# Kernel optimization log

Hardware: AMD Instinct MI355X
Metric: run time of the kernel (lower is better)

The kernel has to match this reference:

```python
import jax, jax.numpy as jnp
import numpy as np

NUM_CLASSES = 19
IGNORE_INDEX = 255
FOCAL_GAMMA = 3.0
FOCAL_WEIGHT = 1.0
EPS = 1e-6


def setup_inputs() -> dict:
    key = jax.random.key(0)
    k1, k2 = jax.random.split(key)
    logits = jax.random.normal(k1, (8, NUM_CLASSES, 512, 512), dtype=jnp.float32)
    targets = jax.random.randint(k2, (8, 512, 512), 0, NUM_CLASSES, dtype=jnp.int64)
    return {"logits": logits, "targets": targets}


def reference(logits, targets):
    C = NUM_CLASSES
    # [B,C,H,W] -> [N,C] log-probs, N = B*H*W
    logp = jax.nn.log_softmax(logits, axis=1)
    lp = jnp.transpose(logp, (0, 2, 3, 1)).reshape(-1, C)
    t = targets.reshape(-1)
    valid = (t != IGNORE_INDEX)
    tc = jnp.clip(t, 0, C - 1)  # safe index for ignored pixels
    validf = valid.astype(lp.dtype)
    n_valid = jnp.maximum(jnp.sum(validf), 1.0)

    # mean cross entropy over valid pixels (F.cross_entropy with ignore_index)
    nll = -jnp.take_along_axis(lp, tc[:, None], axis=1)[:, 0]
    ce = jnp.sum(nll * validf) / n_valid

    # per-class focal term: -log(p_t) * (1 - p_t)^gamma, p_t clamped to [1e-6, 1]
    pt = jnp.clip(jnp.exp(-nll), EPS, 1.0)
    focal_terms = -jnp.log(pt) * (1.0 - pt) ** FOCAL_GAMMA

    # single-pass segment reduce: per-class sum and count over valid pixels
    sums = jax.ops.segment_sum(focal_terms * validf, tc, num_segments=C)
    counts = jax.ops.segment_sum(validf, tc, num_segments=C)
    present = counts > 0
    per_class_mean = sums / jnp.maximum(counts, 1.0)
    n_present = jnp.maximum(jnp.sum(present.astype(lp.dtype)), 1.0)
    focal = jnp.sum(jnp.where(present, per_class_mean, 0.0)) / n_present

    return ce + FOCAL_WEIGHT * focal
```

## Files before the change

kernel.cpp:

```cpp
#include <hip/hip_runtime.h>


#define NCLS 19
#define IGNORE_IDX 255
#define HW4 65536
#define FOCAL_EPS 1e-6f
#define NBLK 2048
#define NQ 40
#define TILE4 128
#define TPIX 512
#define SLOTS (NCLS*TILE4)

__global__ __launch_bounds__(256) void focal_main(
        const float* __restrict__ logits,
        const int*   __restrict__ targets,
        float* __restrict__ P) {
    __shared__ float    lds[NCLS * TPIX];
    __shared__ float    s_csum[NCLS];
    __shared__ unsigned s_ccnt[NCLS];
    __shared__ float    s_wnll[4];
    __shared__ int      s_wcnt[4];

    const int tid = threadIdx.x;
    if (tid < NCLS) { s_csum[tid] = 0.0f; s_ccnt[tid] = 0u; }

    float nll_acc = 0.0f;
    int   vcnt    = 0;

    for (int tt = 0; tt < 2; ++tt) {
        const int tile = blockIdx.x * 2 + tt;
        const int b    = tile >> 9;
        const int tq   = (tile & 511) * TILE4;
        const float4* ibase = reinterpret_cast<const float4*>(logits)
                              + (size_t)b * (NCLS * (size_t)HW4) + tq;

#pragma unroll
        for (int it = 0; it < 10; ++it) {
            const int slot = it * 256 + tid;
            if (slot < SLOTS) {
                const int c   = slot >> 7;
                const int off = slot & 127;
                const float4* src = ibase + (size_t)c * HW4 + off;
                __builtin_amdgcn_global_load_lds(
                    (const __attribute__((address_space(1))) unsigned*)src,
                    (__attribute__((address_space(3))) unsigned*)
                        ((char*)lds + (size_t)slot * 16),
                    16, 0, 0);
            }
        }
        __syncthreads();

        const int pixbase = tile * TPIX;
#pragma unroll
        for (int h = 0; h < 2; ++h) {
            const int pix = tid + h * 256;
            const int t   = targets[pixbase + pix];
            const int tc  = min(max(t, 0), NCLS - 1);
            const bool valid = (t != IGNORE_IDX);

            float s = 0.0f, xt = 0.0f;
#pragma unroll
            for (int c = 0; c < NCLS; ++c) {
                const float v = lds[c * TPIX + pix];
                s += __expf(v);
                if (c == tc) xt = v;
            }
            const float lse = __logf(s);
            const float nll = lse - xt;

            float pt = __expf(-nll);
            pt = fminf(fmaxf(pt, FOCAL_EPS), 1.0f);
            const float om = 1.0f - pt;
            const float f  = -__logf(pt) * om * om * om;

            if (valid) {
                nll_acc += nll; ++vcnt;
                atomicAdd(&s_csum[tc], f);
                atomicAdd(&s_ccnt[tc], 1u);
            }
        }
        __syncthreads();
    }

#pragma unroll
    for (int off = 32; off > 0; off >>= 1) {
        nll_acc += __shfl_down(nll_acc, off);
        vcnt    += __shfl_down(vcnt, off);
    }
    const int wid = tid >> 6, lane = tid & 63;
    if (lane == 0) { s_wnll[wid] = nll_acc; s_wcnt[wid] = vcnt; }
    __syncthreads();

    const unsigned bid = blockIdx.x;
    if (tid == 0) {
        float bn = s_wnll[0] + s_wnll[1] + s_wnll[2] + s_wnll[3];
        int   bc = s_wcnt[0] + s_wcnt[1] + s_wcnt[2] + s_wcnt[3];
        P[0 * NBLK + bid] = bn;
        P[1 * NBLK + bid] = (float)bc;
    }
    if (tid < NCLS) {
        P[(2 + tid) * NBLK + bid]        = s_csum[tid];
        P[(2 + NCLS + tid) * NBLK + bid] = (float)s_ccnt[tid];
    }
}

__global__ __launch_bounds__(1024) void focal_final(
        const float* __restrict__ P, float* __restrict__ out) {
    __shared__ double s_q[NQ];
    const int tid  = threadIdx.x;
    const int wid  = tid >> 6;
    const int lane = tid & 63;

    for (int q = wid; q < NQ; q += 16) {
        double v = 0.0;
#pragma unroll
        for (int k = 0; k < NBLK / 64; ++k)
            v += (double)P[q * NBLK + lane + 64 * k];
#pragma unroll
        for (int off = 32; off > 0; off >>= 1)
            v += __shfl_down(v, off);
        if (lane == 0) s_q[q] = v;
    }
    __syncthreads();

    if (tid == 0) {
        double nv = s_q[1];
        if (nv < 1.0) nv = 1.0;
        const double ce = s_q[0] / nv;

        double fsum = 0.0, npres = 0.0;
        for (int c = 0; c < NCLS; ++c) {
            const double cnt = s_q[2 + NCLS + c];
            if (cnt > 0.0) {
                fsum += s_q[2 + c] / (cnt < 1.0 ? 1.0 : cnt);
                npres += 1.0;
            }
        }
        if (npres < 1.0) npres = 1.0;
        out[0] = (float)(ce + fsum / npres);
    }
}

extern "C" void kernel_launch(void* const* d_in, const int* in_sizes, int n_in,
                              void* d_out, int out_size, void* d_ws, size_t ws_size,
                              hipStream_t stream) {
    const float* logits  = (const float*)d_in[0];
    const int*   targets = (const int*)d_in[1];
    float*       out     = (float*)d_out;
    float*       P       = (float*)d_ws;

    focal_main<<<NBLK, 256, 0, stream>>>(logits, targets, P);
    focal_final<<<1, 1024, 0, stream>>>(P, out);
}
```

Baseline: 235.7 us.

## Double-buffer LDS tiles to overlap async global loads with compute

Each block now processes four smaller tiles of 256 pixels through two LDS buffers, previously two tiles of 512 pixels through one. The async global-to-LDS load of the next tile is issued before the current tile is computed, hiding load latency behind the softmax and focal math. LDS use stays the same, but tiles are smaller and there are more barriers per block. The loop relies on the next tile's async load being complete after the single barrier that ends each iteration, with no explicit wait on outstanding loads.

```diff
diff --git a/kernel.cpp b/kernel.cpp
--- a/kernel.cpp
+++ b/kernel.cpp
@@ -7,15 +7,34 @@
 #define FOCAL_EPS 1e-6f
 #define NBLK 2048
 #define NQ 40
-#define TILE4 128
-#define TPIX 512
+#define TILE4 64
+#define TPIX 256
 #define SLOTS (NCLS*TILE4)
+#define NTILE 4
+
+__device__ __forceinline__ void stage_tile(const float4* __restrict__ tbase,
+                                           float* dst, int tid) {
+#pragma unroll
+    for (int it = 0; it < 5; ++it) {
+        const int slot = it * 256 + tid;
+        if (slot < SLOTS) {
+            const int c   = slot >> 6;
+            const int off = slot & 63;
+            const float4* src = tbase + (size_t)c * HW4 + off;
+            __builtin_amdgcn_global_load_lds(
+                (const __attribute__((address_space(1))) unsigned*)src,
+                (__attribute__((address_space(3))) unsigned*)
+                    ((char*)dst + (size_t)slot * 16),
+                16, 0, 0);
+        }
+    }
+}
 
 __global__ __launch_bounds__(256) void focal_main(
         const float* __restrict__ logits,
         const int*   __restrict__ targets,
         float* __restrict__ P) {
-    __shared__ float    lds[NCLS * TPIX];
+    __shared__ float    lds[2][NCLS * TPIX];
     __shared__ float    s_csum[NCLS];
     __shared__ unsigned s_ccnt[NCLS];
     __shared__ float    s_wnll[4];
@@ -24,61 +43,51 @@
     const int tid = threadIdx.x;
     if (tid < NCLS) { s_csum[tid] = 0.0f; s_ccnt[tid] = 0u; }
 
+    const int tile0 = blockIdx.x * NTILE;
+    const int b     = tile0 >> 10;
+    const float4* plane = reinterpret_cast<const float4*>(logits)
+                          + (size_t)b * (NCLS * (size_t)HW4);
+
+    stage_tile(plane + (size_t)(tile0 & 1023) * TILE4, lds[0], tid);
+    __syncthreads();
+
     float nll_acc = 0.0f;
     int   vcnt    = 0;
 
-    for (int tt = 0; tt < 2; ++tt) {
-        const int tile = blockIdx.x * 2 + tt;
-        const int b    = tile >> 9;
-        const int tq   = (tile & 511) * TILE4;
-        const float4* ibase = reinterpret_cast<const float4*>(logits)
-                              + (size_t)b * (NCLS * (size_t)HW4) + tq;
+#pragma unroll
+    for (int t = 0; t < NTILE; ++t) {
+        const int buf = t & 1;
 
+        if (t + 1 < NTILE)
+            stage_tile(plane + (size_t)((tile0 + t + 1) & 1023) * TILE4,
+                       lds[buf ^ 1], tid);
+
+        const int gpix = (tile0 + t) * TPIX + tid;
+        const int tt   = targets[gpix];
+        const int tc   = min(max(tt, 0), NCLS - 1);
+        const bool valid = (tt != IGNORE_IDX);
+
+        float s = 0.0f, xt = 0.0f;
 #pragma unroll
-        for (int it = 0; it < 10; ++it) {
-            const int slot = it * 256 + tid;
-            if (slot < SLOTS) {
-                const int c   = slot >> 7;
-                const int off = slot & 127;
-                const float4* src = ibase + (size_t)c * HW4 + off;
-                __builtin_amdgcn_global_load_lds(
-                    (const __attribute__((address_space(1))) unsigned*)src,
-                    (__attribute__((address_space(3))) unsigned*)
-                        ((char*)lds + (size_t)slot * 16),
-                    16, 0, 0);
-            }
+        for (int c = 0; c < NCLS; ++c) {
+            const float v = lds[buf][c * TPIX + tid];
+            s += __expf(v);
+            if (c == tc) xt = v;
         }
-        __syncthreads();
+        const float lse = __logf(s);
+        const float nll = lse - xt;
 
-        const int pixbase = tile * TPIX;
-#pragma unroll
-        for (int h = 0; h < 2; ++h) {
-            const int pix = tid + h * 256;
-            const int t   = targets[pixbase + pix];
-            const int tc  = min(max(t, 0), NCLS - 1);
-            const bool valid = (t != IGNORE_IDX);
+        float pt = __expf(-nll);
+        pt = fminf(fmaxf(pt, FOCAL_EPS), 1.0f);
+        const float om = 1.0f - pt;
+        const float f  = -__logf(pt) * om * om * om;
 
-            float s = 0.0f, xt = 0.0f;
-#pragma unroll
-            for (int c = 0; c < NCLS; ++c) {
-                const float v = lds[c * TPIX + pix];
-                s += __expf(v);
-                if (c == tc) xt = v;
-            }
-            const float lse = __logf(s);
-            const float nll = lse - xt;
+        if (valid) {
+            nll_acc += nll; ++vcnt;
+            atomicAdd(&s_csum[tc], f);
+            atomicAdd(&s_ccnt[tc], 1u);
+        }
 
-            float pt = __expf(-nll);
-            pt = fminf(fmaxf(pt, FOCAL_EPS), 1.0f);
-            const float om = 1.0f - pt;
-            const float f  = -__logf(pt) * om * om * om;
-
-            if (valid) {
-                nll_acc += nll; ++vcnt;
-                atomicAdd(&s_csum[tc], f);
-                atomicAdd(&s_ccnt[tc], 1u);
-            }
-        }
         __syncthreads();
     }
 
```

Result: no change. 235.0 us (-0.3%).
